# Kernel tuning notes

Hardware: AMD Instinct MI355X
Metric: run time of the kernel (lower is better)

The kernel has to match this reference:

```python
import jax, jax.numpy as jnp
import numpy as np

KERNEL_SIGMA2 = 4096.0  # = 2 * x_dim, assumed Gaussian RBF kernel

B, K, D, H, Z = 512, 32, 2048, 512, 64


def setup_inputs() -> dict:
    key = jax.random.key(0)
    ks = jax.random.split(key, 8)
    s = lambda k, shp, fan: jax.random.normal(k, shp, jnp.float32) / np.sqrt(fan)
    return {
        "x_c": jax.random.normal(ks[0], (B, D), jnp.float32),
        "x_nn": jax.random.normal(ks[1], (B, K, D), jnp.float32),
        "W1": s(ks[2], (D, H), D), "b1": jnp.zeros((H,), jnp.float32),
        "W2": s(ks[3], (H, Z), H), "b2": jnp.zeros((Z,), jnp.float32),
        "V1": s(ks[4], (Z, H), Z), "c1": jnp.zeros((H,), jnp.float32),
        "V2": s(ks[5], (H, D), H), "c2": jnp.zeros((D,), jnp.float32),
    }


def _enc(x, W1, b1, W2, b2):
    return jax.nn.relu(x @ W1 + b1) @ W2 + b2


def _dec(z, V1, c1, V2, c2):
    return jax.nn.relu(z @ V1 + c1) @ V2 + c2


def reference(x_c, x_nn, W1, b1, W2, b2, V1, c1, V2, c2):
    bs, num_nn, x_dim = x_nn.shape
    z_c = _enc(x_c, W1, b1, W2, b2)                       # [B, Z]
    z_dim = z_c.shape[1]
    z_nn = _enc(x_nn.reshape(bs * num_nn, x_dim), W1, b1, W2, b2)
    z_nn = z_nn.reshape(bs, num_nn, z_dim)
    dz = z_nn - z_c[:, None, :]                           # [B, K, Z]

    # first-order Taylor: recon(z_c) + J(z_c) @ dz via JVP of decoder
    dec_fn = lambda z: _dec(z, V1, c1, V2, c2)
    inputs = jnp.broadcast_to(z_c[:, None, :], (bs, num_nn, z_dim)).reshape(-1, z_dim)
    _, Jdz = jax.jvp(dec_fn, (inputs,), (dz.reshape(-1, z_dim),))  # [B*K, D]

    recon = dec_fn(z_c)                                   # [B, D]
    n_recon = recon[:, None, :] + Jdz.reshape(bs, num_nn, x_dim)

    diff = x_nn - n_recon
    n_loss = jnp.sum(diff * diff, axis=2)                 # ||.||^2, [B, K]
    w = jnp.exp(-jnp.sum((x_nn - x_c[:, None, :]) ** 2, axis=2) / KERNEL_SIGMA2)
    return jnp.mean(w * n_loss)
```

## Files before the change

### kernel.cpp

```cpp
#include <hip/hip_runtime.h>
#include <hip/hip_bf16.h>
#include <cstdint>
#include <cstddef>

#define DEV __device__ __forceinline__

typedef __bf16 bf16;
typedef __bf16 bf16x8 __attribute__((ext_vector_type(8)));
typedef float f32x4 __attribute__((ext_vector_type(4)));

DEV f32x4 mfma16(bf16x8 a, bf16x8 b, f32x4 c) {
  return __builtin_amdgcn_mfma_f32_16x16x32_bf16(a, b, c, 0, 0, 0);
}

DEV void glds16(const void* g, void* l) {
  __builtin_amdgcn_global_load_lds(
      (const __attribute__((address_space(1))) void*)g,
      (__attribute__((address_space(3))) void*)l, 16, 0, 0);
}

template<int ROWS, int NT, int RB>
DEV void stage_tile(const bf16* __restrict__ src, int ld, int row0, int k0,
                    unsigned char* lds, int tid) {
  constexpr int CALLS = (ROWS * RB) / (NT * 16);
  const int wid = tid >> 6, lane = tid & 63;
#pragma unroll
  for (int c = 0; c < CALLS; ++c) {
    const int obase = c * (NT * 16) + wid * 1024;
    const int o = obase + lane * 16;
    const int row = o / RB;
    const int scb = (o & (RB - 1)) ^ ((row & 7) << 4);
    glds16(src + (size_t)(row0 + row) * ld + k0 + (scb >> 1), lds + obase);
  }
}

template<int BM, int BN, int WM, int WN, int MODE, int BK = 64, int MINW = 2>
__global__ __launch_bounds__(WM*WN*64, MINW) void gemm_kernel(
    const bf16* __restrict__ A, const float* __restrict__ Af,
    const float* __restrict__ Af2,
    const bf16* __restrict__ Bt, const float* __restrict__ bias,
    int M, int N, int K,
    float* __restrict__ out32, bf16* __restrict__ out16,
    const float* __restrict__ hc, const float* __restrict__ recon,
    float* __restrict__ nloss, float* __restrict__ warg)
{
  constexpr int NT = WM * WN * 64;
  constexpr int FM = (BM / WM) / 16;
  constexpr int FN = (BN / WN) / 16;
  constexpr int RB = BK * 2;
  constexpr int KH = BK / 32;
  __shared__ __align__(16) unsigned char smem[(BM + BN) * RB];

  const int tid = threadIdx.x, lane = tid & 63, wid = tid >> 6;
  const int wm = wid / WN, wn = wid % WN;
  const int wm0 = wm * (BM / WM), wn0 = wn * (BN / WN);

  int bx = blockIdx.x, by = blockIdx.y;
  {
    const int gx = gridDim.x;
    const int nwg = gx * gridDim.y;
    if ((nwg & 7) == 0) {
      const int fid = by * gx + bx;
      const int cpx = nwg >> 3;
      const int w = (fid & 7) * cpx + (fid >> 3);
      bx = w % gx; by = w / gx;
    }
  }
  const int i0 = by * BM, j0 = bx * BN;
  const int l15 = lane & 15, lg = lane >> 4;

  f32x4 acc[FM][FN] = {};

  int arow[FM], brow[FN];
#pragma unroll
  for (int mi = 0; mi < FM; ++mi) arow[mi] = wm0 + mi * 16 + l15;
#pragma unroll
  for (int ni = 0; ni < FN; ++ni) brow[ni] = wn0 + ni * 16 + l15;

  auto compute = [&](const unsigned char* cA, const unsigned char* cB) {
#pragma unroll
    for (int kh = 0; kh < KH; ++kh) {
      const int koff = kh * 64 + lg * 16;
      bf16x8 af[FM], bfr[FN];
#pragma unroll
      for (int mi = 0; mi < FM; ++mi) {
        const int off = (arow[mi] * RB + koff) ^ ((arow[mi] & 7) << 4);
        af[mi] = *reinterpret_cast<const bf16x8*>(cA + off);
      }
#pragma unroll
      for (int ni = 0; ni < FN; ++ni) {
        const int off = (brow[ni] * RB + koff) ^ ((brow[ni] & 7) << 4);
        bfr[ni] = *reinterpret_cast<const bf16x8*>(cB + off);
      }
#pragma unroll
      for (int mi = 0; mi < FM; ++mi)
#pragma unroll
        for (int ni = 0; ni < FN; ++ni)
          acc[mi][ni] = mfma16(af[mi], bfr[ni], acc[mi][ni]);
    }
  };

  for (int kt = 0; kt < K; kt += BK) {
    stage_tile<BM, NT, RB>(A, K, i0, kt, smem, tid);
    stage_tile<BN, NT, RB>(Bt, K, j0, kt, smem + BM * RB, tid);
    __syncthreads();
    compute(smem, smem + BM * RB);
    __syncthreads();
  }

  if constexpr (MODE == 5) {
    float* eb = (float*)smem;
#pragma unroll
    for (int mi = 0; mi < FM; ++mi) {
      __syncthreads();
#pragma unroll
      for (int ni = 0; ni < FN; ++ni) {
        const int col = wn0 + ni * 16 + l15;
        const int lr0 = wm * 16 + lg * 4;
#pragma unroll
        for (int r = 0; r < 4; ++r)
          eb[(lr0 + r) * 132 + col] = acc[mi][ni][r];
      }
      __syncthreads();
      const int lrow = tid >> 3;
      const int c0 = (tid & 7) * 16;
      const int grow = i0 + (lrow >> 4) * 64 + mi * 16 + (lrow & 15);
      const int b = grow >> 5;
      const float* xp = Af2  + (size_t)grow * 2048 + j0 + c0;
      const float* cp = Af   + (size_t)b * 2048 + j0 + c0;
      const float* rp = recon + (size_t)b * 2048 + j0 + c0;
      float nl = 0.f, wa = 0.f;
#pragma unroll
      for (int q4 = 0; q4 < 4; ++q4) {
        const float4 xv = *(const float4*)(xp + q4 * 4);
        const float4 cv = *(const float4*)(cp + q4 * 4);
        const float4 rv = *(const float4*)(rp + q4 * 4);
#pragma unroll
        for (int q = 0; q < 4; ++q) {
          const float xf = ((const float*)&xv)[q];
          const float d = xf - ((const float*)&rv)[q] - eb[lrow * 132 + c0 + q4 * 4 + q];
          nl += d * d;
          const float wd = xf - ((const float*)&cv)[q];
          wa += wd * wd;
        }
      }
      nl += __shfl_xor(nl, 1, 64); wa += __shfl_xor(wa, 1, 64);
      nl += __shfl_xor(nl, 2, 64); wa += __shfl_xor(wa, 2, 64);
      nl += __shfl_xor(nl, 4, 64); wa += __shfl_xor(wa, 4, 64);
      if ((tid & 7) == 0) {
        atomicAdd(&nloss[grow], nl);
        atomicAdd(&warg[grow], wa);
      }
    }
  } else {
#pragma unroll
    for (int mi = 0; mi < FM; ++mi) {
#pragma unroll
      for (int ni = 0; ni < FN; ++ni) {
#pragma unroll
        for (int r = 0; r < 4; ++r) {
          const int row = i0 + wm0 + mi * 16 + lg * 4 + r;
          const int col = j0 + wn0 + ni * 16 + l15;
          float v = acc[mi][ni][r];
          if constexpr (MODE == 0) {
            v += bias[col];
            out16[(size_t)row * N + col] = (bf16)fmaxf(v, 0.f);
          } else if constexpr (MODE == 1) {
            v += bias[col];
            out32[(size_t)row * N + col] = v;
          } else if constexpr (MODE == 2) {
            v += bias[col];
            out32[(size_t)row * N + col] = v;
            out16[(size_t)row * N + col] = (bf16)fmaxf(v, 0.f);
          } else if constexpr (MODE == 4) {
            const int b = row >> 5;
            const float m = hc[(size_t)b * 512 + col];
            out16[(size_t)row * N + col] = (bf16)(m > 0.f ? v : 0.f);
          }
        }
      }
    }
  }
}

__global__ void cast_x_kernel(const float* __restrict__ x_c,
                              const float* __restrict__ x_nn,
                              bf16* __restrict__ xb) {
  const size_t i = ((size_t)blockIdx.x * 256 + threadIdx.x) * 8;
  constexpr size_t XC = (size_t)512 * 2048;
  const float* s = (i < XC) ? x_c + i : x_nn + (i - XC);
  const float4 a = *(const float4*)s;
  const float4 b = *(const float4*)(s + 4);
  bf16x8 v;
  v[0] = (bf16)a.x; v[1] = (bf16)a.y; v[2] = (bf16)a.z; v[3] = (bf16)a.w;
  v[4] = (bf16)b.x; v[5] = (bf16)b.y; v[6] = (bf16)b.z; v[7] = (bf16)b.w;
  *(bf16x8*)(xb + i) = v;
}

__global__ void transpose_all_kernel(
    const float* __restrict__ W1, const float* __restrict__ W2,
    const float* __restrict__ V1, const float* __restrict__ V2,
    bf16* __restrict__ W1t, bf16* __restrict__ W2t,
    bf16* __restrict__ V1t, bf16* __restrict__ V2t) {
  int blk = blockIdx.x;
  const float* src; bf16* dst; int R, C, gx;
  if (blk < 1024)      { src = W1; dst = W1t; R = 2048; C = 512;  gx = 16; }
  else if (blk < 1056) { blk -= 1024; src = W2; dst = W2t; R = 512; C = 64;   gx = 2;  }
  else if (blk < 1088) { blk -= 1056; src = V1; dst = V1t; R = 64;  C = 512;  gx = 16; }
  else                 { blk -= 1088; src = V2; dst = V2t; R = 512; C = 2048; gx = 64; }
  __shared__ float t[32][33];
  const int c0 = (blk % gx) * 32, r0 = (blk / gx) * 32;
  const int tx = threadIdx.x, ty = threadIdx.y;
#pragma unroll
  for (int i = 0; i < 32; i += 8)
    t[ty + i][tx] = src[(size_t)(r0 + ty + i) * C + c0 + tx];
  __syncthreads();
#pragma unroll
  for (int i = 0; i < 32; i += 8)
    dst[(size_t)(c0 + ty + i) * R + r0 + tx] = (bf16)t[tx][ty + i];
}

__global__ void dz_prep_kernel(const float* __restrict__ z,
                               bf16* __restrict__ dzb,
                               bf16* __restrict__ zcb,
                               float* __restrict__ nw,
                               float* __restrict__ out) {
  const int i = blockIdx.x * 256 + threadIdx.x;
  if (i < 32768) nw[i] = 0.f;
  if (i == 0) out[0] = 0.f;
  const int r = i >> 6, j = i & 63;
  const float v = z[i];
  if (r < 512) {
    zcb[i] = (bf16)v;
  } else {
    const int rn = r - 512;
    const int b = rn >> 5;
    dzb[(size_t)rn * 64 + j] = (bf16)(v - z[(size_t)b * 64 + j]);
  }
}

__global__ void finalize_kernel(const float* __restrict__ nloss,
                                const float* __restrict__ warg,
                                float* __restrict__ out) {
  const int i = blockIdx.x * 256 + threadIdx.x;
  float v = expf(-warg[i] * (1.0f / 4096.0f)) * nloss[i] * (1.0f / 16384.0f);
#pragma unroll
  for (int s = 1; s < 64; s <<= 1) v += __shfl_xor(v, s, 64);
  __shared__ float red[4];
  const int lane = threadIdx.x & 63, w = threadIdx.x >> 6;
  if (lane == 0) red[w] = v;
  __syncthreads();
  if (threadIdx.x == 0) atomicAdd(out, red[0] + red[1] + red[2] + red[3]);
}

extern "C" void kernel_launch(void* const* d_in, const int* in_sizes, int n_in,
                              void* d_out, int out_size, void* d_ws, size_t ws_size,
                              hipStream_t stream) {
  const float* x_c = (const float*)d_in[0];
  const float* x_nn = (const float*)d_in[1];
  const float* W1 = (const float*)d_in[2];
  const float* b1 = (const float*)d_in[3];
  const float* W2 = (const float*)d_in[4];
  const float* b2 = (const float*)d_in[5];
  const float* V1 = (const float*)d_in[6];
  const float* c1 = (const float*)d_in[7];
  const float* V2 = (const float*)d_in[8];
  const float* c2 = (const float*)d_in[9];
  float* out = (float*)d_out;
  char* ws = (char*)d_ws;

  size_t off = 0;
  auto take = [&](size_t n) { size_t o = off; off += n; return o; };
  bf16*  W1t   = (bf16*) (ws + take((size_t)512 * 2048 * 2));
  bf16*  W2t   = (bf16*) (ws + take((size_t)64 * 512 * 2));
  bf16*  V1t   = (bf16*) (ws + take((size_t)512 * 64 * 2));
  bf16*  V2t   = (bf16*) (ws + take((size_t)2048 * 512 * 2));
  bf16*  h1    = (bf16*) (ws + take((size_t)16896 * 512 * 2));
  float* z     = (float*)(ws + take((size_t)16896 * 64 * 4));
  bf16*  dzb   = (bf16*) (ws + take((size_t)16384 * 64 * 2));
  bf16*  zcb   = (bf16*) (ws + take((size_t)512 * 64 * 2));
  float* hc    = (float*)(ws + take((size_t)512 * 512 * 4));
  bf16*  acb   = (bf16*) (ws + take((size_t)512 * 512 * 2));
  float* recon = (float*)(ws + take((size_t)512 * 2048 * 4));
  bf16*  dab   = (bf16*) (ws + take((size_t)16384 * 512 * 2));
  float* nloss = (float*)(ws + take((size_t)16384 * 4));
  float* warg  = (float*)(ws + take((size_t)16384 * 4));
  bf16*  xb    = (bf16*) (ws + take((size_t)16896 * 2048 * 2));

  cast_x_kernel<<<dim3(16896), dim3(256), 0, stream>>>(x_c, x_nn, xb);

  transpose_all_kernel<<<dim3(2112), dim3(32, 8), 0, stream>>>(
      W1, W2, V1, V2, W1t, W2t, V1t, V2t);

  gemm_kernel<128, 128, 2, 2, 0, 128><<<dim3(4, 132), dim3(256), 0, stream>>>(
      xb, nullptr, nullptr, W1t, b1, 16896, 512, 2048,
      nullptr, h1, nullptr, nullptr, nullptr, nullptr);

  gemm_kernel<64, 64, 2, 2, 1><<<dim3(1, 264), dim3(256), 0, stream>>>(
      h1, nullptr, nullptr, W2t, b2, 16896, 64, 512,
      z, nullptr, nullptr, nullptr, nullptr, nullptr);

  dz_prep_kernel<<<dim3(4224), dim3(256), 0, stream>>>(z, dzb, zcb, nloss, out);

  gemm_kernel<128, 128, 2, 2, 2><<<dim3(4, 4), dim3(256), 0, stream>>>(
      zcb, nullptr, nullptr, V1t, c1, 512, 512, 64,
      hc, acb, nullptr, nullptr, nullptr, nullptr);

  gemm_kernel<64, 128, 2, 2, 1><<<dim3(16, 8), dim3(256), 0, stream>>>(
      acb, nullptr, nullptr, V2t, c2, 512, 2048, 512,
      recon, nullptr, nullptr, nullptr, nullptr, nullptr);

  gemm_kernel<128, 128, 2, 2, 4><<<dim3(4, 128), dim3(256), 0, stream>>>(
      dzb, nullptr, nullptr, V1t, nullptr, 16384, 512, 64,
      nullptr, dab, hc, nullptr, nullptr, nullptr);

  gemm_kernel<128, 128, 2, 2, 5><<<dim3(16, 128), dim3(256), 0, stream>>>(
      dab, x_c, x_nn, V2t, nullptr, 16384, 2048, 512,
      nullptr, nullptr, nullptr, recon, nloss, warg);

  finalize_kernel<<<dim3(64), dim3(256), 0, stream>>>(nloss, warg, out);
}
```

Before: 189.8 us.

## Split-K the first encoder GEMM into four chunks with a separate reduction kernel

The large x@W1 GEMM (16896x512x2048) is split along K into four z-slices, each writing fp32 partials to a new workspace buffer. A new reduce kernel sums the four partials, adds the bias, applies ReLU and casts to bf16 for h1. This raises the block count from 528 to 2112 so more CUs stay busy. The cost is writing and re-reading about 138 MB of fp32 partials plus one extra launch, and BK also drops from 128 to 64.

```diff
diff --git a/kernel.cpp b/kernel.cpp
--- a/kernel.cpp
+++ b/kernel.cpp
@@ -34,7 +34,8 @@
   }
 }
 
-template<int BM, int BN, int WM, int WN, int MODE, int BK = 64, int MINW = 2>
+template<int BM, int BN, int WM, int WN, int MODE, int BK = 64,
+         int KCHUNKS = 1, int MINW = 2>
 __global__ __launch_bounds__(WM*WN*64, MINW) void gemm_kernel(
     const bf16* __restrict__ A, const float* __restrict__ Af,
     const float* __restrict__ Af2,
@@ -100,7 +101,9 @@
     }
   };
 
-  for (int kt = 0; kt < K; kt += BK) {
+  const int kcn = K / KCHUNKS;
+  const int kb = (KCHUNKS > 1) ? (int)blockIdx.z * kcn : 0;
+  for (int kt = kb; kt < kb + kcn; kt += BK) {
     stage_tile<BM, NT, RB>(A, K, i0, kt, smem, tid);
     stage_tile<BN, NT, RB>(Bt, K, j0, kt, smem + BM * RB, tid);
     __syncthreads();
@@ -176,11 +179,43 @@
             const int b = row >> 5;
             const float m = hc[(size_t)b * 512 + col];
             out16[(size_t)row * N + col] = (bf16)(m > 0.f ? v : 0.f);
+          } else if constexpr (MODE == 6) {
+            out32[(size_t)blockIdx.z * M * N + (size_t)row * N + col] = v;
           }
         }
       }
     }
   }
+}
+
+__global__ void reduce_h1_kernel(const float* __restrict__ hp,
+                                 const float* __restrict__ b1,
+                                 bf16* __restrict__ h1) {
+  constexpr size_t MN = (size_t)16896 * 512;
+  const size_t i = ((size_t)blockIdx.x * 256 + threadIdx.x) * 8;
+  const int col = (int)(i & 511);
+  float s[8];
+  {
+    const float4 a0 = *(const float4*)(hp + i);
+    const float4 a1 = *(const float4*)(hp + i + 4);
+    s[0] = a0.x; s[1] = a0.y; s[2] = a0.z; s[3] = a0.w;
+    s[4] = a1.x; s[5] = a1.y; s[6] = a1.z; s[7] = a1.w;
+  }
+#pragma unroll
+  for (int c = 1; c < 4; ++c) {
+    const float* p = hp + c * MN + i;
+    const float4 a0 = *(const float4*)p;
+    const float4 a1 = *(const float4*)(p + 4);
+    s[0] += a0.x; s[1] += a0.y; s[2] += a0.z; s[3] += a0.w;
+    s[4] += a1.x; s[5] += a1.y; s[6] += a1.z; s[7] += a1.w;
+  }
+  const float4 b0 = *(const float4*)(b1 + col);
+  const float4 b1v = *(const float4*)(b1 + col + 4);
+  const float bb[8] = {b0.x, b0.y, b0.z, b0.w, b1v.x, b1v.y, b1v.z, b1v.w};
+  bf16x8 v;
+#pragma unroll
+  for (int q = 0; q < 8; ++q) v[q] = (bf16)fmaxf(s[q] + bb[q], 0.f);
+  *(bf16x8*)(h1 + i) = v;
 }
 
 __global__ void cast_x_kernel(const float* __restrict__ x_c,
@@ -286,15 +321,18 @@
   float* nloss = (float*)(ws + take((size_t)16384 * 4));
   float* warg  = (float*)(ws + take((size_t)16384 * 4));
   bf16*  xb    = (bf16*) (ws + take((size_t)16896 * 2048 * 2));
+  float* hp    = (float*)(ws + take((size_t)4 * 16896 * 512 * 4));
 
   cast_x_kernel<<<dim3(16896), dim3(256), 0, stream>>>(x_c, x_nn, xb);
 
   transpose_all_kernel<<<dim3(2112), dim3(32, 8), 0, stream>>>(
       W1, W2, V1, V2, W1t, W2t, V1t, V2t);
 
-  gemm_kernel<128, 128, 2, 2, 0, 128><<<dim3(4, 132), dim3(256), 0, stream>>>(
-      xb, nullptr, nullptr, W1t, b1, 16896, 512, 2048,
-      nullptr, h1, nullptr, nullptr, nullptr, nullptr);
+  gemm_kernel<128, 128, 2, 2, 6, 64, 4><<<dim3(4, 132, 4), dim3(256), 0, stream>>>(
+      xb, nullptr, nullptr, W1t, nullptr, 16896, 512, 2048,
+      hp, nullptr, nullptr, nullptr, nullptr, nullptr);
+
+  reduce_h1_kernel<<<dim3(4224), dim3(256), 0, stream>>>(hp, b1, h1);
 
   gemm_kernel<64, 64, 2, 2, 1><<<dim3(1, 264), dim3(256), 0, stream>>>(
       h1, nullptr, nullptr, W2t, b2, 16896, 64, 512,
```

After: 231.2 us. 21.8% more time.
